# Kernel tuning notes

Hardware: AMD Instinct MI355X
Metric: run time of the kernel (lower is better)

## Reference

```python
import jax, jax.numpy as jnp
import numpy as np

B, S, DIM = 2, 2048, 2048
N_HEADS, N_KV_HEADS = 16, 4
HEAD_DIM = DIM // N_HEADS  # 128
N_REP = N_HEADS // N_KV_HEADS  # 4


def setup_inputs() -> dict:
    key = jax.random.key(0)
    ks = jax.random.split(key, 7)
    x = jax.random.normal(ks[0], (B, S, DIM), dtype=jnp.float32)
    cos = jax.random.uniform(ks[1], (S, HEAD_DIM // 2), dtype=jnp.float32)
    sin = jax.random.uniform(ks[2], (S, HEAD_DIM // 2), dtype=jnp.float32)
    sc = 1.0 / np.sqrt(DIM)
    wq = jax.random.normal(ks[3], (DIM, N_HEADS * HEAD_DIM), dtype=jnp.float32) * sc
    wk = jax.random.normal(ks[4], (DIM, N_KV_HEADS * HEAD_DIM), dtype=jnp.float32) * sc
    wv = jax.random.normal(ks[5], (DIM, N_KV_HEADS * HEAD_DIM), dtype=jnp.float32) * sc
    wo = jax.random.normal(ks[6], (N_HEADS * HEAD_DIM, DIM), dtype=jnp.float32) * sc
    return {"x": x, "cos": cos, "sin": sin, "wq": wq, "wk": wk, "wv": wv, "wo": wo}


def _rope(t, cos, sin):
    # t: [B, S, H, hd]; cos/sin: [S, hd/2] -> broadcast as [1, S, 1, hd/2]
    tr, ti = t[..., ::2], t[..., 1::2]
    c = cos[None, :, None, :]
    s = sin[None, :, None, :]
    out_r = tr * c - ti * s
    out_i = tr * s + ti * c
    # interleave back: stack on new last axis then flatten
    return jnp.stack([out_r, out_i], axis=-1).reshape(t.shape)


def reference(x, cos, sin, wq, wk, wv, wo):
    bsz, seqlen, _ = x.shape
    xq = (x @ wq).reshape(bsz, seqlen, N_HEADS, HEAD_DIM)
    xk = (x @ wk).reshape(bsz, seqlen, N_KV_HEADS, HEAD_DIM)
    xv = (x @ wv).reshape(bsz, seqlen, N_KV_HEADS, HEAD_DIM)
    xq = _rope(xq, cos, sin)
    xk = _rope(xk, cos, sin)
    # GQA: repeat kv heads -> [B, S, H, hd]
    xk = jnp.repeat(xk, N_REP, axis=2)
    xv = jnp.repeat(xv, N_REP, axis=2)
    scale = 1.0 / jnp.sqrt(jnp.asarray(HEAD_DIM, dtype=x.dtype))
    scores = jnp.einsum("bqhd,bkhd->bhqk", xq, xk) * scale
    causal = jnp.tril(jnp.ones((seqlen, seqlen), dtype=bool))
    scores = jnp.where(causal[None, None, :, :], scores, jnp.asarray(-jnp.inf, dtype=scores.dtype))
    attn = jax.nn.softmax(scores, axis=-1)
    out = jnp.einsum("bhqk,bkhd->bqhd", attn, xv)
    out = out.reshape(bsz, seqlen, N_HEADS * HEAD_DIM)
    return out @ wo
```

## Files before the change

### kernel.cpp

```cpp
#include <hip/hip_runtime.h>
#include <stdint.h>

#define SEQ 2048

typedef uint16_t u16;
typedef uint32_t u32;
typedef __attribute__((ext_vector_type(4))) float f32x4;
typedef __attribute__((ext_vector_type(8))) __bf16 bf16x8;
typedef __attribute__((ext_vector_type(4))) __bf16 bf16x4;

__device__ __forceinline__ u16 f2bf(float f) {
    u32 u = __float_as_uint(f);
    u += 0x7FFFu + ((u >> 16) & 1u);
    return (u16)(u >> 16);
}
__device__ __forceinline__ float bf2f(u16 h) {
    return __uint_as_float(((u32)h) << 16);
}
__device__ __forceinline__ void async16(const void* g, void* l) {
    auto gp = (__attribute__((address_space(1))) void*)const_cast<void*>(g);
    auto lp = (__attribute__((address_space(3))) void*)l;
    __builtin_amdgcn_global_load_lds(gp, lp, 16, 0, 0);
}

__global__ __launch_bounds__(256) void convert_bf16(const float* __restrict__ src,
                                                    u16* __restrict__ dst) {
    int i = blockIdx.x * 256 + threadIdx.x;
    float4 v = ((const float4*)src)[i];
    u32 lo = (u32)f2bf(v.x) | ((u32)f2bf(v.y) << 16);
    u32 hi = (u32)f2bf(v.z) | ((u32)f2bf(v.w) << 16);
    ((uint2*)dst)[i] = make_uint2(lo, hi);
}

__global__ __launch_bounds__(256) void tconv(const float* __restrict__ src,
                                             u16* __restrict__ dst, int N, int K) {
    __shared__ float tile[64][65];
    const int n0 = blockIdx.x * 64, k0 = blockIdx.y * 64;
    const int tid = threadIdx.x;
#pragma unroll
    for (int p = 0; p < 4; p++) {
        int r = p * 16 + (tid >> 4);
        int c = (tid & 15) * 4;
        float4 v = *(const float4*)&src[(size_t)(k0 + r) * N + n0 + c];
        tile[r][c] = v.x; tile[r][c+1] = v.y; tile[r][c+2] = v.z; tile[r][c+3] = v.w;
    }
    __syncthreads();
#pragma unroll
    for (int p = 0; p < 4; p++) {
        int n = p * 16 + (tid >> 4);
        int kq = (tid & 15) * 4;
        u32 lo = (u32)f2bf(tile[kq+0][n]) | ((u32)f2bf(tile[kq+1][n]) << 16);
        u32 hi = (u32)f2bf(tile[kq+2][n]) | ((u32)f2bf(tile[kq+3][n]) << 16);
        *(uint2*)&dst[(size_t)(n0 + n) * K + k0 + kq] = make_uint2(lo, hi);
    }
}

template <bool F32OUT>
__global__ __launch_bounds__(256) void gemm128(const u16* __restrict__ A,
                                               const u16* __restrict__ Bt,
                                               void* __restrict__ Cv,
                                               int M, int N, int K) {
    __shared__ u16 lA[128 * 32];
    __shared__ u16 lB[128 * 32];
    const int tid = threadIdx.x;
    const int m0 = blockIdx.y * 128, n0 = blockIdx.x * 128;
    const int lane = tid & 63;
    const int lr = lane & 15, quad = lane >> 4;
    const int w = tid >> 6;
    const int wm = (w >> 1) * 64, wn = (w & 1) * 64;

    f32x4 acc[4][4] = {};

    const int srow = tid >> 2;
    const int schunk = (tid & 3) ^ (srow & 3);
    const u16* aS0 = A  + (size_t)(m0 + srow) * K + schunk * 8;
    const u16* aS1 = aS0 + (size_t)64 * K;
    const u16* bS0 = Bt + (size_t)(n0 + srow) * K + schunk * 8;
    const u16* bS1 = bS0 + (size_t)64 * K;
    u16* lAd = lA + tid * 8;
    u16* lBd = lB + tid * 8;

    for (int k0 = 0; k0 < K; k0 += 32) {
        __syncthreads();
        async16(aS0 + k0, lAd);
        async16(aS1 + k0, lAd + 2048);
        async16(bS0 + k0, lBd);
        async16(bS1 + k0, lBd + 2048);
        __syncthreads();
        bf16x8 af[4], bfr[4];
        const int cs = (quad ^ (lr & 3)) * 8;
#pragma unroll
        for (int i = 0; i < 4; i++)
            af[i] = *(const bf16x8*)&lA[(wm + i * 16 + lr) * 32 + cs];
#pragma unroll
        for (int i = 0; i < 4; i++)
            bfr[i] = *(const bf16x8*)&lB[(wn + i * 16 + lr) * 32 + cs];
#pragma unroll
        for (int mf = 0; mf < 4; mf++)
#pragma unroll
            for (int nf = 0; nf < 4; nf++)
                acc[mf][nf] = __builtin_amdgcn_mfma_f32_16x16x32_bf16(
                    af[mf], bfr[nf], acc[mf][nf], 0, 0, 0);
    }

#pragma unroll
    for (int mf = 0; mf < 4; mf++) {
#pragma unroll
        for (int nf = 0; nf < 4; nf++) {
#pragma unroll
            for (int r = 0; r < 4; r++) {
                size_t row = (size_t)(m0 + wm + mf * 16 + quad * 4 + r);
                size_t col = (size_t)(n0 + wn + nf * 16 + lr);
                if (F32OUT)
                    ((float*)Cv)[row * (size_t)N + col] = acc[mf][nf][r];
                else
                    ((u16*)Cv)[row * (size_t)N + col] = f2bf(acc[mf][nf][r]);
            }
        }
    }
}

__global__ __launch_bounds__(256) void rope_k(u16* __restrict__ qkv,
                                              const float* __restrict__ cosp,
                                              const float* __restrict__ sinp) {
    const int t = blockIdx.x;
    const int spos = t & (SEQ - 1);
    const int tid = threadIdx.x;
    u16* row = qkv + (size_t)t * 3072;
    const int col = 2048 + 2 * tid;
    const int ci = tid & 63;
    u32 v = *(u32*)(row + col);
    float tr = bf2f((u16)(v & 0xFFFFu));
    float ti = bf2f((u16)(v >> 16));
    float cs = cosp[spos * 64 + ci];
    float sn = sinp[spos * 64 + ci];
    float orr = tr * cs - ti * sn;
    float oi  = tr * sn + ti * cs;
    *(u32*)(row + col) = (u32)f2bf(orr) | ((u32)f2bf(oi) << 16);
}

__global__ __launch_bounds__(256) void transpose_v(const u16* __restrict__ qkv,
                                                   u16* __restrict__ vt) {
    __shared__ u16 tile[64][65];
    const int bid = blockIdx.x;
    const int dt = bid & 1;
    const int st = (bid >> 1) & 31;
    const int kh = (bid >> 6) & 3;
    const int b  = bid >> 8;
    const int tid = threadIdx.x;
#pragma unroll
    for (int pp = 0; pp < 2; pp++) {
        int r  = pp * 32 + (tid >> 3);
        int c8 = (tid & 7) * 8;
        const u16* src = qkv + (size_t)(b * SEQ + st * 64 + r) * 3072 + 2560 + kh * 128 + dt * 64 + c8;
        uint4 v = *(const uint4*)src;
        tile[r][c8+0] = (u16)(v.x & 0xFFFF); tile[r][c8+1] = (u16)(v.x >> 16);
        tile[r][c8+2] = (u16)(v.y & 0xFFFF); tile[r][c8+3] = (u16)(v.y >> 16);
        tile[r][c8+4] = (u16)(v.z & 0xFFFF); tile[r][c8+5] = (u16)(v.z >> 16);
        tile[r][c8+6] = (u16)(v.w & 0xFFFF); tile[r][c8+7] = (u16)(v.w >> 16);
    }
    __syncthreads();
#pragma unroll
    for (int pp = 0; pp < 2; pp++) {
        int dr = pp * 32 + (tid >> 3);
        int s8 = (tid & 7) * 8;
        uint4 o;
        o.x = (u32)tile[s8+0][dr] | ((u32)tile[s8+1][dr] << 16);
        o.y = (u32)tile[s8+2][dr] | ((u32)tile[s8+3][dr] << 16);
        o.z = (u32)tile[s8+4][dr] | ((u32)tile[s8+5][dr] << 16);
        o.w = (u32)tile[s8+6][dr] | ((u32)tile[s8+7][dr] << 16);
        u16* dst = vt + ((size_t)((b * 4 + kh) * 128 + dt * 64 + dr)) * SEQ + st * 64 + s8;
        *(uint4*)dst = o;
    }
}

__global__ __launch_bounds__(512, 2) void flash_attn(const u16* __restrict__ qkv,
                                                     const u16* __restrict__ vt,
                                                     const float* __restrict__ cosp,
                                                     const float* __restrict__ sinp,
                                                     u16* __restrict__ ob) {
    __shared__ u16 sh[49152];
    const int bidx = blockIdx.x;
    const int a  = bidx & 7;
    const int bh = bidx >> 3;
    const int b = bh >> 4, h = bh & 15, kh = h >> 2;
    const int tid = threadIdx.x;
    const int w = tid >> 6, lane = tid & 63;
    const int grp = w >> 2, wl = w & 3;
    const int lr = lane & 15, quad = lane >> 4;
    const float qscale = 0.088388347762f * 1.4426950408889634f;

    u16* lKg = sh + grp * 16384;
    u16* lVg = lKg + 8192;
    u16* lPw = sh + 32768 + w * 2048;

    const int tidg = tid & 255;
    const int krow = tidg >> 4;
    const int kchunk = (tidg & 15) ^ krow;
    const int vrow = tidg >> 3;
    const int vchunk = (tidg & 7) ^ (vrow & 7);
    const u16* kRow = qkv + (size_t)b * SEQ * 3072 + 2048 + kh * 128
                    + (size_t)krow * 3072 + kchunk * 8;
    const u16* vRow = vt + (size_t)(b * 4 + kh) * 128 * SEQ
                    + (size_t)vrow * SEQ + vchunk * 8;
    u16* lKd = lKg + tidg * 8;
    u16* lVd = lVg + tidg * 8;

    float* mO = (float*)sh;
    float* mM = (float*)(sh + 32768);

    for (int p = 0; p < 2; p++) {
        const int qt = p ? (7 - a) : (8 + a);
        const int niters = p ? (8 - a) : (9 + a);
        const int kt0 = grp * niters;

        bf16x8 qf[2][4];
#pragma unroll
        for (int qi = 0; qi < 2; qi++) {
            const int token = qt * 128 + wl * 32 + qi * 16 + lr;
            const u16* qb = qkv + (size_t)(b * SEQ + token) * 3072 + h * 128;
#pragma unroll
            for (int kk = 0; kk < 4; kk++) {
                uint4 raw = *(const uint4*)(qb + kk * 32 + quad * 8);
                u32 rw[4] = {raw.x, raw.y, raw.z, raw.w};
                union { u16 us[8]; bf16x8 v; } fr;
#pragma unroll
                for (int pp = 0; pp < 4; pp++) {
                    int ci = kk * 16 + quad * 4 + pp;
                    float cv = cosp[token * 64 + ci];
                    float sv = sinp[token * 64 + ci];
                    float tr = bf2f((u16)(rw[pp] & 0xFFFFu));
                    float ti = bf2f((u16)(rw[pp] >> 16));
                    fr.us[2 * pp]     = f2bf((tr * cv - ti * sv) * qscale);
                    fr.us[2 * pp + 1] = f2bf((tr * sv + ti * cv) * qscale);
                }
                qf[qi][kk] = fr.v;
            }
        }

        f32x4 o[2][8] = {};
        float m_st[2] = {-1e30f, -1e30f};
        float l_st[2] = {0.f, 0.f};
        const int qg = qt * 128 + wl * 32 + lr;

        for (int t = 0; t < niters; t++) {
            const int kt = kt0 + t;
#pragma unroll
            for (int i = 0; i < 4; i++)
                async16(kRow + (size_t)(kt * 64 + i * 16) * 3072, lKd + i * 2048);
#pragma unroll
            for (int i = 0; i < 4; i++)
                async16(vRow + (size_t)(i * 32) * SEQ + kt * 64, lVd + i * 2048);
            asm volatile("s_waitcnt vmcnt(0)" ::: "memory");
            asm volatile("s_barrier" ::: "memory");

            f32x4 sc[2][4] = {};
#pragma unroll
            for (int nf = 0; nf < 4; nf++) {
#pragma unroll
                for (int kk = 0; kk < 4; kk++) {
                    bf16x8 ak = *(const bf16x8*)&lKg[(nf * 16 + lr) * 128 + (((kk * 4 + quad) ^ lr) * 8)];
                    sc[0][nf] = __builtin_amdgcn_mfma_f32_16x16x32_bf16(ak, qf[0][kk], sc[0][nf], 0, 0, 0);
                    sc[1][nf] = __builtin_amdgcn_mfma_f32_16x16x32_bf16(ak, qf[1][kk], sc[1][nf], 0, 0, 0);
                }
            }

            const int kb = kt * 64 + quad * 4;
#pragma unroll
            for (int qi = 0; qi < 2; qi++) {
                float ps[4][4];
                float mnew = m_st[qi];
                const int qrow_g = qg + qi * 16;
#pragma unroll
                for (int nf = 0; nf < 4; nf++)
#pragma unroll
                    for (int r = 0; r < 4; r++) {
                        float v = sc[qi][nf][r];
                        if ((kb + nf * 16 + r) > qrow_g) v = -1e30f;
                        ps[nf][r] = v;
                        mnew = fmaxf(mnew, v);
                    }
                mnew = fmaxf(mnew, __shfl_xor(mnew, 16));
                mnew = fmaxf(mnew, __shfl_xor(mnew, 32));
                float rsum = 0.f;
#pragma unroll
                for (int nf = 0; nf < 4; nf++)
#pragma unroll
                    for (int r = 0; r < 4; r++) {
                        float e = exp2f(ps[nf][r] - mnew);
                        ps[nf][r] = e;
                        rsum += e;
                    }
                rsum += __shfl_xor(rsum, 16);
                rsum += __shfl_xor(rsum, 32);
                float alpha = exp2f(m_st[qi] - mnew);
                l_st[qi] = l_st[qi] * alpha + rsum;
                m_st[qi] = mnew;
#pragma unroll
                for (int r = 0; r < 4; r++) {
                    float ar = __shfl(alpha, quad * 4 + r, 16);
#pragma unroll
                    for (int nd = 0; nd < 8; nd++) o[qi][nd][r] *= ar;
                }
                const int qrow = qi * 16 + lr;
#pragma unroll
                for (int nf = 0; nf < 4; nf++) {
                    u32 lo = (u32)f2bf(ps[nf][0]) | ((u32)f2bf(ps[nf][1]) << 16);
                    u32 hi = (u32)f2bf(ps[nf][2]) | ((u32)f2bf(ps[nf][3]) << 16);
                    int c = (nf * 4 + quad) ^ lr;
                    *(uint2*)&lPw[qrow * 64 + c * 4] = make_uint2(lo, hi);
                }
            }

#pragma unroll
            for (int kf = 0; kf < 2; kf++) {
                bf16x8 pa[2];
#pragma unroll
                for (int qi = 0; qi < 2; qi++) {
                    int c0 = (kf * 8 + quad * 2) ^ lr;
                    int c1 = (kf * 8 + quad * 2 + 1) ^ lr;
                    bf16x4 p0 = *(const bf16x4*)&lPw[(qi * 16 + lr) * 64 + c0 * 4];
                    bf16x4 p1 = *(const bf16x4*)&lPw[(qi * 16 + lr) * 64 + c1 * 4];
                    pa[qi] = __builtin_shufflevector(p0, p1, 0, 1, 2, 3, 4, 5, 6, 7);
                }
#pragma unroll
                for (int nd = 0; nd < 8; nd++) {
                    bf16x8 vb = *(const bf16x8*)&lVg[(nd * 16 + lr) * 64 + (((kf * 4 + quad) ^ (lr & 7)) * 8)];
                    o[0][nd] = __builtin_amdgcn_mfma_f32_16x16x32_bf16(pa[0], vb, o[0][nd], 0, 0, 0);
                    o[1][nd] = __builtin_amdgcn_mfma_f32_16x16x32_bf16(pa[1], vb, o[1][nd], 0, 0, 0);
                }
            }

            asm volatile("s_barrier" ::: "memory");
        }

        __syncthreads();
        if (grp == 1) {
#pragma unroll
            for (int qi = 0; qi < 2; qi++) {
#pragma unroll
                for (int r = 0; r < 4; r++) {
                    int row = wl * 32 + qi * 16 + quad * 4 + r;
#pragma unroll
                    for (int nd = 0; nd < 8; nd++)
                        mO[row * 128 + nd * 16 + lr] = o[qi][nd][r];
                }
                if (quad == 0) {
                    int rowl = wl * 32 + qi * 16 + lr;
                    mM[rowl * 2]     = m_st[qi];
                    mM[rowl * 2 + 1] = l_st[qi];
                }
            }
        }
        __syncthreads();
        if (grp == 0) {
#pragma unroll
            for (int qi = 0; qi < 2; qi++) {
                int rowl = wl * 32 + qi * 16 + lr;
                float m1 = mM[rowl * 2], l1 = mM[rowl * 2 + 1];
                float M  = fmaxf(m_st[qi], m1);
                float a0 = exp2f(m_st[qi] - M);
                float a1 = exp2f(m1 - M);
                float li = 1.0f / (l_st[qi] * a0 + l1 * a1);
                u16* obase = ob + (size_t)(b * SEQ + qt * 128 + wl * 32 + qi * 16) * 2048 + h * 128;
#pragma unroll
                for (int r = 0; r < 4; r++) {
                    float a0b = __shfl(a0, quad * 4 + r, 16);
                    float a1b = __shfl(a1, quad * 4 + r, 16);
                    float lib = __shfl(li, quad * 4 + r, 16);
                    int row = wl * 32 + qi * 16 + quad * 4 + r;
#pragma unroll
                    for (int nd = 0; nd < 8; nd++) {
                        float val = (o[qi][nd][r] * a0b + mO[row * 128 + nd * 16 + lr] * a1b) * lib;
                        obase[(quad * 4 + r) * 2048 + nd * 16 + lr] = f2bf(val);
                    }
                }
            }
        }
        __syncthreads();
    }
}

extern "C" void kernel_launch(void* const* d_in, const int* in_sizes, int n_in,
                              void* d_out, int out_size, void* d_ws, size_t ws_size,
                              hipStream_t stream) {
    (void)in_sizes; (void)n_in; (void)out_size; (void)ws_size;
    const float* x    = (const float*)d_in[0];
    const float* cosp = (const float*)d_in[1];
    const float* sinp = (const float*)d_in[2];
    const float* wq   = (const float*)d_in[3];
    const float* wk   = (const float*)d_in[4];
    const float* wv   = (const float*)d_in[5];
    const float* wo   = (const float*)d_in[6];
    float* out = (float*)d_out;

    char* ws = (char*)d_ws;
    u16* xb    = (u16*)(ws);
    u16* qkvb  = (u16*)(ws + (size_t)16 * 1024 * 1024);
    u16* wqkvT = (u16*)(ws + (size_t)40 * 1024 * 1024);
    u16* woT   = (u16*)(ws + (size_t)52 * 1024 * 1024);
    u16* vtb   = (u16*)(ws + (size_t)60 * 1024 * 1024);
    u16* ob    = xb;

    convert_bf16<<<8192, 256, 0, stream>>>(x, xb);
    tconv<<<dim3(32, 32), 256, 0, stream>>>(wq, wqkvT, 2048, 2048);
    tconv<<<dim3( 8, 32), 256, 0, stream>>>(wk, wqkvT + (size_t)2048 * 2048, 512, 2048);
    tconv<<<dim3( 8, 32), 256, 0, stream>>>(wv, wqkvT + (size_t)2560 * 2048, 512, 2048);
    tconv<<<dim3(32, 32), 256, 0, stream>>>(wo, woT, 2048, 2048);
    gemm128<false><<<dim3(24, 32), 256, 0, stream>>>(xb, wqkvT, (void*)qkvb, 4096, 3072, 2048);
    rope_k<<<4096, 256, 0, stream>>>(qkvb, cosp, sinp);
    transpose_v<<<512, 256, 0, stream>>>(qkvb, vtb);
    flash_attn<<<256, 512, 0, stream>>>(qkvb, vtb, cosp, sinp, ob);
    gemm128<true><<<dim3(16, 32), 256, 0, stream>>>(ob, woT, (void*)out, 4096, 2048, 2048);
}
```

Before: 336.7 us.

## Use 256-row multi-stage pipelined GEMM with XCD remap and lazy softmax rescale

Replaces the 128x128 single-buffered GEMM with a 256xBN tile, 512-thread kernel that keeps a 4-slot LDS ring, prefetching three k-steps ahead. It uses fine-grained vmcnt waits, s_setprio around the MFMA bursts, and remaps block IDs so neighbouring tiles share an XCD. The goal is to hide global load latency and raise arithmetic intensity in the QKV and output projections. Flash attention now skips causal masking for tiles that lie fully below the diagonal, and only rescales the running max and accumulator when the new max exceeds the old one by more than a threshold. The lazy rescale saves exp and multiply work but allows exponents above 1 (up to 2^8 per tile), which bounds precision and overflow headroom.

```diff
diff --git a/kernel.cpp b/kernel.cpp
--- a/kernel.cpp
+++ b/kernel.cpp
@@ -55,66 +55,146 @@
     }
 }
 
-template <bool F32OUT>
-__global__ __launch_bounds__(256) void gemm128(const u16* __restrict__ A,
-                                               const u16* __restrict__ Bt,
-                                               void* __restrict__ Cv,
-                                               int M, int N, int K) {
-    __shared__ u16 lA[128 * 32];
-    __shared__ u16 lB[128 * 32];
+template <int BN, bool F32OUT>
+__global__ __launch_bounds__(512, 2) void gemm256(const u16* __restrict__ A,
+                                                  const u16* __restrict__ Bt,
+                                                  void* __restrict__ Cv,
+                                                  int N, int K, int nbx) {
+    constexpr int NF = BN / 64;
+    constexpr int SLOT = 8192 + BN * 32;
+    __shared__ u16 lds[4 * SLOT];
+
+    const int nwg = gridDim.x;
+    const int q = nwg >> 3, r = nwg & 7;
+    const int xcd = blockIdx.x & 7, lid = blockIdx.x >> 3;
+    const int wg = (xcd < r ? xcd * (q + 1) : r * (q + 1) + (xcd - r) * q) + lid;
+    const int by = wg / nbx, bx = wg - by * nbx;
+    const int m0 = by * 256, n0 = bx * BN;
+
     const int tid = threadIdx.x;
-    const int m0 = blockIdx.y * 128, n0 = blockIdx.x * 128;
-    const int lane = tid & 63;
-    const int lr = lane & 15, quad = lane >> 4;
-    const int w = tid >> 6;
-    const int wm = (w >> 1) * 64, wn = (w & 1) * 64;
-
-    f32x4 acc[4][4] = {};
-
-    const int srow = tid >> 2;
-    const int schunk = (tid & 3) ^ (srow & 3);
-    const u16* aS0 = A  + (size_t)(m0 + srow) * K + schunk * 8;
-    const u16* aS1 = aS0 + (size_t)64 * K;
-    const u16* bS0 = Bt + (size_t)(n0 + srow) * K + schunk * 8;
-    const u16* bS1 = bS0 + (size_t)64 * K;
-    u16* lAd = lA + tid * 8;
-    u16* lBd = lB + tid * 8;
-
-    for (int k0 = 0; k0 < K; k0 += 32) {
-        __syncthreads();
-        async16(aS0 + k0, lAd);
-        async16(aS1 + k0, lAd + 2048);
-        async16(bS0 + k0, lBd);
-        async16(bS1 + k0, lBd + 2048);
-        __syncthreads();
-        bf16x8 af[4], bfr[4];
-        const int cs = (quad ^ (lr & 3)) * 8;
-#pragma unroll
-        for (int i = 0; i < 4; i++)
-            af[i] = *(const bf16x8*)&lA[(wm + i * 16 + lr) * 32 + cs];
-#pragma unroll
-        for (int i = 0; i < 4; i++)
-            bfr[i] = *(const bf16x8*)&lB[(wn + i * 16 + lr) * 32 + cs];
-#pragma unroll
-        for (int mf = 0; mf < 4; mf++)
-#pragma unroll
-            for (int nf = 0; nf < 4; nf++)
-                acc[mf][nf] = __builtin_amdgcn_mfma_f32_16x16x32_bf16(
-                    af[mf], bfr[nf], acc[mf][nf], 0, 0, 0);
-    }
-
-#pragma unroll
-    for (int mf = 0; mf < 4; mf++) {
-#pragma unroll
-        for (int nf = 0; nf < 4; nf++) {
-#pragma unroll
-            for (int r = 0; r < 4; r++) {
-                size_t row = (size_t)(m0 + wm + mf * 16 + quad * 4 + r);
+    const int w = tid >> 6, l = tid & 63;
+    const int lr = l & 15, quad = l >> 4;
+    const int wm = (w >> 2) * 128;
+    const int wn = (w & 3) * (BN / 4);
+    const int cs = (quad ^ (lr & 3)) * 8;
+
+    const int rA = w * 32 + (l >> 2);
+    const int gA = ((l & 3) ^ (rA & 3)) * 8;
+    const u16* aS = A + (size_t)(m0 + rA) * K + gA;
+    u16* ldA = lds + (w * 128 + l) * 8;
+
+    const u16* bS;
+    u16* ldB;
+    if constexpr (BN == 256) {
+        bS = Bt + (size_t)(n0 + rA) * K + gA;
+        ldB = lds + 8192 + (w * 128 + l) * 8;
+    } else {
+        const int rB = w * 16 + (l >> 2);
+        const int gB = ((l & 3) ^ (rB & 3)) * 8;
+        bS = Bt + (size_t)(n0 + rB) * K + gB;
+        ldB = lds + 8192 + tid * 8;
+    }
+
+    f32x4 acc[8][NF] = {};
+    const int nK = K >> 5;
+
+    auto stageA = [&](int kt) {
+        u16* d = ldA + (kt & 3) * SLOT;
+        const u16* s = aS + (size_t)kt * 32;
+        async16(s, d);
+        async16(s + (size_t)16 * K, d + 512);
+    };
+    auto stageB = [&](int kt) {
+        u16* d = ldB + (kt & 3) * SLOT;
+        const u16* s = bS + (size_t)kt * 32;
+        async16(s, d);
+        if constexpr (BN == 256) async16(s + (size_t)16 * K, d + 512);
+    };
+
+    stageA(0); stageB(0); stageA(1); stageB(1); stageA(2); stageB(2);
+    if constexpr (BN == 256)
+        asm volatile("s_waitcnt vmcnt(8)" ::: "memory");
+    else
+        asm volatile("s_waitcnt vmcnt(6)" ::: "memory");
+    __builtin_amdgcn_s_barrier();
+
+    for (int kt = 0; kt < nK; ++kt) {
+        const u16* As = lds + (kt & 3) * SLOT;
+        const u16* Bs = As + 8192;
+        const bool pre = (kt + 3 < nK);
+        if constexpr (BN == 256) {
+            bf16x8 af[4], bfr[4];
+#pragma unroll
+            for (int i = 0; i < 4; i++)
+                af[i] = *(const bf16x8*)&As[(wm + i * 16 + lr) * 32 + cs];
+#pragma unroll
+            for (int i = 0; i < 4; i++)
+                bfr[i] = *(const bf16x8*)&Bs[(wn + i * 16 + lr) * 32 + cs];
+            if (pre) stageA(kt + 3);
+            __builtin_amdgcn_s_barrier();
+            asm volatile("s_waitcnt lgkmcnt(0)" ::: "memory");
+            __builtin_amdgcn_s_setprio(1);
+#pragma unroll
+            for (int mf = 0; mf < 4; mf++)
+#pragma unroll
+                for (int nf = 0; nf < 4; nf++)
+                    acc[mf][nf] = __builtin_amdgcn_mfma_f32_16x16x32_bf16(af[mf], bfr[nf], acc[mf][nf], 0, 0, 0);
+            __builtin_amdgcn_s_setprio(0);
+            __builtin_amdgcn_s_barrier();
+#pragma unroll
+            for (int i = 0; i < 4; i++)
+                af[i] = *(const bf16x8*)&As[(wm + 64 + i * 16 + lr) * 32 + cs];
+            if (pre) stageB(kt + 3);
+            __builtin_amdgcn_s_barrier();
+            asm volatile("s_waitcnt lgkmcnt(0)" ::: "memory");
+            __builtin_amdgcn_s_setprio(1);
+#pragma unroll
+            for (int mf = 0; mf < 4; mf++)
+#pragma unroll
+                for (int nf = 0; nf < 4; nf++)
+                    acc[4 + mf][nf] = __builtin_amdgcn_mfma_f32_16x16x32_bf16(af[mf], bfr[nf], acc[4 + mf][nf], 0, 0, 0);
+            __builtin_amdgcn_s_setprio(0);
+            if (kt < nK - 3)       asm volatile("s_waitcnt vmcnt(8)" ::: "memory");
+            else if (kt == nK - 3) asm volatile("s_waitcnt vmcnt(4)" ::: "memory");
+            else if (kt == nK - 2) asm volatile("s_waitcnt vmcnt(0)" ::: "memory");
+            if (kt < nK - 1) __builtin_amdgcn_s_barrier();
+        } else {
+            bf16x8 af[8], bfr[2];
+#pragma unroll
+            for (int i = 0; i < 8; i++)
+                af[i] = *(const bf16x8*)&As[(wm + i * 16 + lr) * 32 + cs];
+#pragma unroll
+            for (int i = 0; i < 2; i++)
+                bfr[i] = *(const bf16x8*)&Bs[(wn + i * 16 + lr) * 32 + cs];
+            if (pre) { stageA(kt + 3); stageB(kt + 3); }
+            __builtin_amdgcn_s_barrier();
+            asm volatile("s_waitcnt lgkmcnt(0)" ::: "memory");
+            __builtin_amdgcn_s_setprio(1);
+#pragma unroll
+            for (int mf = 0; mf < 8; mf++)
+#pragma unroll
+                for (int nf = 0; nf < 2; nf++)
+                    acc[mf][nf] = __builtin_amdgcn_mfma_f32_16x16x32_bf16(af[mf], bfr[nf], acc[mf][nf], 0, 0, 0);
+            __builtin_amdgcn_s_setprio(0);
+            if (kt < nK - 3)       asm volatile("s_waitcnt vmcnt(6)" ::: "memory");
+            else if (kt == nK - 3) asm volatile("s_waitcnt vmcnt(3)" ::: "memory");
+            else if (kt == nK - 2) asm volatile("s_waitcnt vmcnt(0)" ::: "memory");
+            if (kt < nK - 1) __builtin_amdgcn_s_barrier();
+        }
+    }
+
+#pragma unroll
+    for (int mf = 0; mf < 8; mf++) {
+#pragma unroll
+        for (int nf = 0; nf < NF; nf++) {
+#pragma unroll
+            for (int rr = 0; rr < 4; rr++) {
+                size_t row = (size_t)(m0 + wm + mf * 16 + quad * 4 + rr);
                 size_t col = (size_t)(n0 + wn + nf * 16 + lr);
                 if (F32OUT)
-                    ((float*)Cv)[row * (size_t)N + col] = acc[mf][nf][r];
+                    ((float*)Cv)[row * (size_t)N + col] = acc[mf][nf][rr];
                 else
-                    ((u16*)Cv)[row * (size_t)N + col] = f2bf(acc[mf][nf][r]);
+                    ((u16*)Cv)[row * (size_t)N + col] = f2bf(acc[mf][nf][rr]);
             }
         }
     }
@@ -266,42 +346,60 @@
             }
 
             const int kb = kt * 64 + quad * 4;
+            const int kmax = kt * 64 + 63;
 #pragma unroll
             for (int qi = 0; qi < 2; qi++) {
                 float ps[4][4];
-                float mnew = m_st[qi];
+                float tmax = -1e30f;
                 const int qrow_g = qg + qi * 16;
+                if (kmax > qt * 128 + wl * 32 + qi * 16) {
+#pragma unroll
+                    for (int nf = 0; nf < 4; nf++)
+#pragma unroll
+                        for (int r = 0; r < 4; r++) {
+                            float v = sc[qi][nf][r];
+                            if ((kb + nf * 16 + r) > qrow_g) v = -1e30f;
+                            ps[nf][r] = v;
+                            tmax = fmaxf(tmax, v);
+                        }
+                } else {
+#pragma unroll
+                    for (int nf = 0; nf < 4; nf++)
+#pragma unroll
+                        for (int r = 0; r < 4; r++) {
+                            float v = sc[qi][nf][r];
+                            ps[nf][r] = v;
+                            tmax = fmaxf(tmax, v);
+                        }
+                }
+                tmax = fmaxf(tmax, __shfl_xor(tmax, 16));
+                tmax = fmaxf(tmax, __shfl_xor(tmax, 32));
+                const float mprev = m_st[qi];
+                if (!__all(tmax - mprev <= 8.0f)) {
+                    float mnew = fmaxf(mprev, tmax);
+                    float alpha = exp2f(mprev - mnew);
+                    l_st[qi] *= alpha;
+                    m_st[qi] = mnew;
+#pragma unroll
+                    for (int r = 0; r < 4; r++) {
+                        float ar = __shfl(alpha, quad * 4 + r, 16);
+#pragma unroll
+                        for (int nd = 0; nd < 8; nd++) o[qi][nd][r] *= ar;
+                    }
+                }
+                const float mcur = m_st[qi];
+                float rsum = 0.f;
 #pragma unroll
                 for (int nf = 0; nf < 4; nf++)
 #pragma unroll
                     for (int r = 0; r < 4; r++) {
-                        float v = sc[qi][nf][r];
-                        if ((kb + nf * 16 + r) > qrow_g) v = -1e30f;
-                        ps[nf][r] = v;
-                        mnew = fmaxf(mnew, v);
-                    }
-                mnew = fmaxf(mnew, __shfl_xor(mnew, 16));
-                mnew = fmaxf(mnew, __shfl_xor(mnew, 32));
-                float rsum = 0.f;
-#pragma unroll
-                for (int nf = 0; nf < 4; nf++)
-#pragma unroll
-                    for (int r = 0; r < 4; r++) {
-                        float e = exp2f(ps[nf][r] - mnew);
+                        float e = exp2f(ps[nf][r] - mcur);
                         ps[nf][r] = e;
                         rsum += e;
                     }
                 rsum += __shfl_xor(rsum, 16);
                 rsum += __shfl_xor(rsum, 32);
-                float alpha = exp2f(m_st[qi] - mnew);
-                l_st[qi] = l_st[qi] * alpha + rsum;
-                m_st[qi] = mnew;
-#pragma unroll
-                for (int r = 0; r < 4; r++) {
-                    float ar = __shfl(alpha, quad * 4 + r, 16);
-#pragma unroll
-                    for (int nd = 0; nd < 8; nd++) o[qi][nd][r] *= ar;
-                }
+                l_st[qi] += rsum;
                 const int qrow = qi * 16 + lr;
 #pragma unroll
                 for (int nf = 0; nf < 4; nf++) {
@@ -407,9 +505,9 @@
     tconv<<<dim3( 8, 32), 256, 0, stream>>>(wk, wqkvT + (size_t)2048 * 2048, 512, 2048);
     tconv<<<dim3( 8, 32), 256, 0, stream>>>(wv, wqkvT + (size_t)2560 * 2048, 512, 2048);
     tconv<<<dim3(32, 32), 256, 0, stream>>>(wo, woT, 2048, 2048);
-    gemm128<false><<<dim3(24, 32), 256, 0, stream>>>(xb, wqkvT, (void*)qkvb, 4096, 3072, 2048);
+    gemm256<256, false><<<192, 512, 0, stream>>>(xb, wqkvT, (void*)qkvb, 3072, 2048, 12);
     rope_k<<<4096, 256, 0, stream>>>(qkvb, cosp, sinp);
     transpose_v<<<512, 256, 0, stream>>>(qkvb, vtb);
     flash_attn<<<256, 512, 0, stream>>>(qkvb, vtb, cosp, sinp, ob);
-    gemm128<true><<<dim3(16, 32), 256, 0, stream>>>(ob, woT, (void*)out, 4096, 2048, 2048);
-}
+    gemm256<128, true><<<256, 512, 0, stream>>>(ob, woT, (void*)out, 2048, 2048, 16);
+}
```

After: 327.8 us. 1.03x faster.
